# Kernel tuning notes

Measured on AMD Instinct MI355X. Metric: run time of the kernel, lower is better.

## Reference

```python
import jax, jax.numpy as jnp
import numpy as np

BATCH = 262144
N_STEPS = 10  # hard-coded `range(10)` in the original get_cycles


def _euler_to_matrix(e):
    # Standard extrinsic xyz convention: R = Rz(z) @ Ry(y) @ Rx(x)
    x, y, z = e[..., 0], e[..., 1], e[..., 2]
    cx, sx = jnp.cos(x), jnp.sin(x)
    cy, sy = jnp.cos(y), jnp.sin(y)
    cz, sz = jnp.cos(z), jnp.sin(z)
    r0 = jnp.stack([cz * cy, cz * sy * sx - sz * cx, cz * sy * cx + sz * sx], -1)
    r1 = jnp.stack([sz * cy, sz * sy * sx + cz * cx, sz * sy * cx - cz * sx], -1)
    r2 = jnp.stack([-sy, cy * sx, cy * cx], -1)
    return jnp.stack([r0, r1, r2], -2)  # (..., 3, 3)


def _matrix_to_euler(R):
    # Classic rotationMatrixToEulerAngles (inverse of Rz@Ry@Rx), with singular branch
    sy = jnp.sqrt(R[..., 0, 0] ** 2 + R[..., 1, 0] ** 2)
    singular = sy < 1e-6
    x = jnp.where(singular,
                  jnp.arctan2(-R[..., 1, 2], R[..., 1, 1]),
                  jnp.arctan2(R[..., 2, 1], R[..., 2, 2]))
    y = jnp.arctan2(-R[..., 2, 0], sy)
    z = jnp.where(singular, jnp.zeros_like(sy), jnp.arctan2(R[..., 1, 0], R[..., 0, 0]))
    return jnp.stack([x, y, z], -1)


def _get_cycles(x):
    # x: (B, 6*N_STEPS), interleaved [t(3), r(3)] per step (per the original reshape())
    x = jax.lax.stop_gradient(x)  # mirrors .detach().numpy() in the original
    g = x.reshape(x.shape[0], N_STEPS, 6)
    t = g[:, :, :3]   # (B, S, 3) translations
    r = g[:, :, 3:]   # (B, S, 3) euler rotations

    # --- translation part ---
    # The original aliases path_pred[0] onto t[0:3] via .numpy() and mutates it
    # in-place across cycle iterations (j=0 doubles it). The resulting recorded
    # values obey: v_0 = t_0 ; v_i = 2*v_{i-1} + sum_{j=1}^{i-1} t_j
    C = jnp.cumsum(t[:, 1:, :], axis=1)  # C[:, k-1, :] = sum_{j=1..k} t_j
    v = [t[:, 0, :]]
    for i in range(1, N_STEPS):
        tail = C[:, i - 2, :] if i >= 2 else jnp.zeros_like(v[0])
        v.append(2.0 * v[-1] + tail)
    trans = jnp.stack(v, axis=1)  # (B, S, 3)

    # --- rotation part ---
    # numpy `*=` is ELEMENTWISE, so cycle i records
    # matrix_to_euler( R(r_1) * prod_{j<i} R(r_j) )  (Hadamard product)
    R = _euler_to_matrix(r)                    # (B, S, 3, 3)
    CP = jnp.cumprod(R, axis=1)                # CP[:, k] = elemwise prod_{j<=k} R_j
    P = jnp.concatenate([jnp.ones_like(R[:, :1]), CP[:, :-1]], axis=1)  # prod_{j<i}
    M = R[:, 1:2] * P                          # (B, S, 3, 3)
    rot = _matrix_to_euler(M)                  # (B, S, 3)

    return jnp.stack([trans, rot], axis=2)     # (B, S, 2, 3)


def setup_inputs():
    key = jax.random.key(0)
    k1, k2 = jax.random.split(key)
    pred = jax.random.normal(k1, (BATCH, 6 * N_STEPS), dtype=jnp.float32)
    gt = jax.random.normal(k2, (BATCH, 6 * N_STEPS), dtype=jnp.float32)
    return {"pred": pred, "gt": gt}


def reference(pred, gt):
    pred_cycles = _get_cycles(pred)
    gt_cycles = _get_cycles(gt)
    loss = jnp.mean((pred_cycles - gt_cycles) ** 2)
    return loss / BATCH  # original divides the MSE by self.batch_size
```

## Files before the change

### kernel.cpp

```cpp
#include <hip/hip_runtime.h>
#include <math.h>

#define NSTEP 10
#define ROWS_PER_BLOCK 128
#define ROW_STRIDE 61
#define HALF_OFF (ROWS_PER_BLOCK * ROW_STRIDE)

__device__ __forceinline__ float fast_atan2f(float y, float x) {
    float ax = fabsf(x), ay = fabsf(y);
    float mx = fmaxf(ax, ay);
    float mn = fminf(ax, ay);
    float a = mn * __builtin_amdgcn_rcpf(fmaxf(mx, 1e-38f));
    float s = a * a;
    float r = fmaf(s, fmaf(s, fmaf(s, fmaf(s, 0.0208351f, -0.085133f),
                                   0.180141f), -0.3302995f), 0.9998660f) * a;
    if (ay > ax) r = 1.57079632679f - r;
    if (x < 0.0f) r = 3.14159265359f - r;
    return copysignf(r, y);
}

__device__ __forceinline__ void euler2mat(float x, float y, float z, float R[9]) {
    float sx, cx, sy, cy, sz, cz;
    __sincosf(x, &sx, &cx);
    __sincosf(y, &sy, &cy);
    __sincosf(z, &sz, &cz);
    R[0] = cz * cy; R[1] = cz * sy * sx - sz * cx; R[2] = cz * sy * cx + sz * sx;
    R[3] = sz * cy; R[4] = sz * sy * sx + cz * cx; R[5] = sz * sy * cx - cz * sx;
    R[6] = -sy;     R[7] = cy * sx;                R[8] = cy * cx;
}

__device__ __forceinline__ void emit(float v, float& acc) {
    int pi = __builtin_amdgcn_update_dpp(0, __float_as_int(v), 0xB1, 0xF, 0xF, true);
    float d = v - __int_as_float(pi);
    acc = fmaf(d, d, acc);
}

__device__ __forceinline__ void emit_euler(const float M[9], float& acc) {
    float sy = sqrtf(fmaf(M[0], M[0], M[3] * M[3]));
    bool sing = sy < 1e-6f;
    float a0 = sing ? -M[5] : M[7];
    float a1 = sing ?  M[4] : M[8];
    emit(fast_atan2f(a0, a1), acc);
    emit(fast_atan2f(-M[6], sy), acc);
    emit(sing ? 0.0f : fast_atan2f(M[3], M[0]), acc);
}

__global__ __launch_bounds__(256) void cycle_loss_main(
    const float* __restrict__ pred, const float* __restrict__ gt,
    float* __restrict__ partial, int batch)
{
    __shared__ float lds[2 * HALF_OFF];
    const int tid = threadIdx.x;

    {
        const size_t gbase = (size_t)blockIdx.x * (ROWS_PER_BLOCK * 60);
        #pragma unroll
        for (int it = 0; it < 30; ++it) {
            int i = tid + it * 256;
            int lidx = i + i / 60;
            lds[lidx]            = pred[gbase + i];
            lds[HALF_OFF + lidx] = gt[gbase + i];
        }
    }
    __syncthreads();

    float acc = 0.0f;
    {
        const float* row = lds + ((tid & 1) ? HALF_OFF : 0) + (tid >> 1) * ROW_STRIDE;

        float v[3], cac[3] = {0,0,0}, tprev[3];
        float Q[9];

        float e0 = row[0], e1 = row[1], e2 = row[2], e3 = row[3];
        float e4 = row[4], e5 = row[5], e6 = row[6], e7 = row[7];
        float e8 = row[8], e9 = row[9], e10 = row[10], e11 = row[11];

        v[0] = e0; v[1] = e1; v[2] = e2;
        emit(v[0], acc); emit(v[1], acc); emit(v[2], acc);
        #pragma unroll
        for (int k = 0; k < 3; ++k) { v[k] *= 2.0f; emit(v[k], acc); }
        tprev[0] = e6; tprev[1] = e7; tprev[2] = e8;

        {
            float R1[9];
            euler2mat(e3, e4, e5, Q);
            euler2mat(e9, e10, e11, R1);
            emit_euler(R1, acc);
            #pragma unroll
            for (int k = 0; k < 9; ++k) Q[k] *= R1[k];
            emit_euler(Q, acc);
            #pragma unroll
            for (int k = 0; k < 9; ++k) Q[k] *= R1[k];
        }

        #pragma unroll
        for (int c = 1; c < 5; ++c) {
            const float* rc = row + 12 * c;
            float f0 = rc[0], f1 = rc[1], f2 = rc[2], f3 = rc[3];
            float f4 = rc[4], f5 = rc[5], f6 = rc[6], f7 = rc[7];
            float f8 = rc[8], f9 = rc[9], f10 = rc[10], f11 = rc[11];

            cac[0] += tprev[0]; cac[1] += tprev[1]; cac[2] += tprev[2];
            #pragma unroll
            for (int k = 0; k < 3; ++k) { v[k] = fmaf(2.0f, v[k], cac[k]); emit(v[k], acc); }
            cac[0] += f0; cac[1] += f1; cac[2] += f2;
            #pragma unroll
            for (int k = 0; k < 3; ++k) { v[k] = fmaf(2.0f, v[k], cac[k]); emit(v[k], acc); }
            tprev[0] = f6; tprev[1] = f7; tprev[2] = f8;

            emit_euler(Q, acc);
            {
                float R[9];
                euler2mat(f3, f4, f5, R);
                #pragma unroll
                for (int k = 0; k < 9; ++k) Q[k] *= R[k];
            }
            emit_euler(Q, acc);
            if (c < 4) {
                float R[9];
                euler2mat(f9, f10, f11, R);
                #pragma unroll
                for (int k = 0; k < 9; ++k) Q[k] *= R[k];
            }
        }
    }

    int lane = tid & 63;
    int wid  = tid >> 6;
    #pragma unroll
    for (int off = 32; off > 0; off >>= 1)
        acc += __shfl_down(acc, off, 64);
    __shared__ float warp_s[4];
    if (lane == 0) warp_s[wid] = acc;
    __syncthreads();
    if (tid == 0)
        partial[blockIdx.x] = warp_s[0] + warp_s[1] + warp_s[2] + warp_s[3];
}

__global__ __launch_bounds__(256) void cycle_loss_fin(
    const float* __restrict__ partial, float* __restrict__ out,
    int nblocks, float inv)
{
    int t = threadIdx.x;
    float s = 0.0f;
    for (int i = t; i < nblocks; i += 256) s += partial[i];
    int lane = t & 63, wid = t >> 6;
    #pragma unroll
    for (int off = 32; off > 0; off >>= 1)
        s += __shfl_down(s, off, 64);
    __shared__ float warp_s[4];
    if (lane == 0) warp_s[wid] = s;
    __syncthreads();
    if (t == 0)
        out[0] = (warp_s[0] + warp_s[1] + warp_s[2] + warp_s[3]) * inv;
}

extern "C" void kernel_launch(void* const* d_in, const int* in_sizes, int n_in,
                              void* d_out, int out_size, void* d_ws, size_t ws_size,
                              hipStream_t stream) {
    const float* pred = (const float*)d_in[0];
    const float* gt   = (const float*)d_in[1];
    int batch = in_sizes[0] / 60;
    float* partial = (float*)d_ws;

    const int threads = 256;
    const int blocks = batch / ROWS_PER_BLOCK;
    cycle_loss_main<<<blocks, threads, 0, stream>>>(pred, gt, partial, batch);

    double inv = 0.5 / (60.0 * (double)batch * (double)batch);
    cycle_loss_fin<<<1, threads, 0, stream>>>(partial, (float*)d_out, blocks, (float)inv);
}
```

Baseline: 145.2 us.

## Stage inputs as packed fp16 in per-wave LDS tiles with float2 loads

Each wave now loads its own 32 rows of pred and gt with float2 global loads and converts them to packed half2 (round-toward-zero) before writing to LDS. This halves LDS footprint and LDS read count and allows more blocks per CU. The block-wide reduction barrier is replaced by per-wave partial sums written to global memory, and the final kernel sums four times as many partials. Storing inputs in fp16 loses precision, which is amplified by the doubling recurrence in the translation path and may break accuracy tolerance.

```diff
diff --git a/kernel.cpp b/kernel.cpp
--- a/kernel.cpp
+++ b/kernel.cpp
@@ -2,9 +2,11 @@
 #include <math.h>
 
 #define NSTEP 10
-#define ROWS_PER_BLOCK 128
-#define ROW_STRIDE 61
-#define HALF_OFF (ROWS_PER_BLOCK * ROW_STRIDE)
+#define ROW_U32 31
+#define GT_OFF  (32 * ROW_U32)
+#define WAVE_U32 (64 * ROW_U32)
+
+typedef __fp16 half2_t __attribute__((ext_vector_type(2)));
 
 __device__ __forceinline__ float fast_atan2f(float y, float x) {
     float ax = fabsf(x), ay = fabsf(y);
@@ -45,35 +47,55 @@
     emit(sing ? 0.0f : fast_atan2f(M[3], M[0]), acc);
 }
 
+__device__ __forceinline__ void unpack2(unsigned u, float& lo, float& hi) {
+    union { unsigned u; half2_t h; } cv; cv.u = u;
+    lo = (float)cv.h.x; hi = (float)cv.h.y;
+}
+
 __global__ __launch_bounds__(256) void cycle_loss_main(
     const float* __restrict__ pred, const float* __restrict__ gt,
-    float* __restrict__ partial, int batch)
+    float* __restrict__ partial)
 {
-    __shared__ float lds[2 * HALF_OFF];
-    const int tid = threadIdx.x;
+    __shared__ unsigned lds[4 * WAVE_U32];
+    const int tid  = threadIdx.x;
+    const int lane = tid & 63;
+    const int wid  = tid >> 6;
 
     {
-        const size_t gbase = (size_t)blockIdx.x * (ROWS_PER_BLOCK * 60);
+        const size_t rbase = ((size_t)blockIdx.x * 128 + wid * 32) * 30;
+        const float2* pp = reinterpret_cast<const float2*>(pred) + rbase;
+        const float2* gp = reinterpret_cast<const float2*>(gt)   + rbase;
+        unsigned* lw = lds + wid * WAVE_U32;
+
+        int cp  = lane % 30;
+        int idx = (lane / 30) * ROW_U32 + cp;
         #pragma unroll
-        for (int it = 0; it < 30; ++it) {
-            int i = tid + it * 256;
-            int lidx = i + i / 60;
-            lds[lidx]            = pred[gbase + i];
-            lds[HALF_OFF + lidx] = gt[gbase + i];
+        for (int it = 0; it < 15; ++it) {
+            float2 a = pp[lane + 64 * it];
+            float2 b = gp[lane + 64 * it];
+            half2_t ha = __builtin_amdgcn_cvt_pkrtz(a.x, a.y);
+            half2_t hb = __builtin_amdgcn_cvt_pkrtz(b.x, b.y);
+            union { half2_t h; unsigned u; } ca, cb; ca.h = ha; cb.h = hb;
+            lw[idx]          = ca.u;
+            lw[GT_OFF + idx] = cb.u;
+            idx += 2 * ROW_U32 + 4; cp += 4;
+            if (cp >= 30) { cp -= 30; idx += 1; }
         }
     }
     __syncthreads();
 
     float acc = 0.0f;
     {
-        const float* row = lds + ((tid & 1) ? HALF_OFF : 0) + (tid >> 1) * ROW_STRIDE;
+        const unsigned* row = lds + wid * WAVE_U32
+                            + ((lane & 1) ? GT_OFF : 0) + (lane >> 1) * ROW_U32;
 
         float v[3], cac[3] = {0,0,0}, tprev[3];
         float Q[9];
 
-        float e0 = row[0], e1 = row[1], e2 = row[2], e3 = row[3];
-        float e4 = row[4], e5 = row[5], e6 = row[6], e7 = row[7];
-        float e8 = row[8], e9 = row[9], e10 = row[10], e11 = row[11];
+        float e0,e1,e2,e3,e4,e5,e6,e7,e8,e9,e10,e11;
+        unpack2(row[0], e0, e1);  unpack2(row[1], e2, e3);
+        unpack2(row[2], e4, e5);  unpack2(row[3], e6, e7);
+        unpack2(row[4], e8, e9);  unpack2(row[5], e10, e11);
 
         v[0] = e0; v[1] = e1; v[2] = e2;
         emit(v[0], acc); emit(v[1], acc); emit(v[2], acc);
@@ -95,10 +117,11 @@
 
         #pragma unroll
         for (int c = 1; c < 5; ++c) {
-            const float* rc = row + 12 * c;
-            float f0 = rc[0], f1 = rc[1], f2 = rc[2], f3 = rc[3];
-            float f4 = rc[4], f5 = rc[5], f6 = rc[6], f7 = rc[7];
-            float f8 = rc[8], f9 = rc[9], f10 = rc[10], f11 = rc[11];
+            const unsigned* rc = row + 6 * c;
+            float f0,f1,f2,f3,f4,f5,f6,f7,f8,f9,f10,f11;
+            unpack2(rc[0], f0, f1);  unpack2(rc[1], f2, f3);
+            unpack2(rc[2], f4, f5);  unpack2(rc[3], f6, f7);
+            unpack2(rc[4], f8, f9);  unpack2(rc[5], f10, f11);
 
             cac[0] += tprev[0]; cac[1] += tprev[1]; cac[2] += tprev[2];
             #pragma unroll
@@ -125,25 +148,20 @@
         }
     }
 
-    int lane = tid & 63;
-    int wid  = tid >> 6;
     #pragma unroll
     for (int off = 32; off > 0; off >>= 1)
         acc += __shfl_down(acc, off, 64);
-    __shared__ float warp_s[4];
-    if (lane == 0) warp_s[wid] = acc;
-    __syncthreads();
-    if (tid == 0)
-        partial[blockIdx.x] = warp_s[0] + warp_s[1] + warp_s[2] + warp_s[3];
+    if (lane == 0)
+        partial[blockIdx.x * 4 + wid] = acc;
 }
 
 __global__ __launch_bounds__(256) void cycle_loss_fin(
     const float* __restrict__ partial, float* __restrict__ out,
-    int nblocks, float inv)
+    int nparts, float inv)
 {
     int t = threadIdx.x;
     float s = 0.0f;
-    for (int i = t; i < nblocks; i += 256) s += partial[i];
+    for (int i = t; i < nparts; i += 256) s += partial[i];
     int lane = t & 63, wid = t >> 6;
     #pragma unroll
     for (int off = 32; off > 0; off >>= 1)
@@ -164,9 +182,9 @@
     float* partial = (float*)d_ws;
 
     const int threads = 256;
-    const int blocks = batch / ROWS_PER_BLOCK;
-    cycle_loss_main<<<blocks, threads, 0, stream>>>(pred, gt, partial, batch);
+    const int blocks = batch / 128;
+    cycle_loss_main<<<blocks, threads, 0, stream>>>(pred, gt, partial);
 
     double inv = 0.5 / (60.0 * (double)batch * (double)batch);
-    cycle_loss_fin<<<1, threads, 0, stream>>>(partial, (float*)d_out, blocks, (float)inv);
+    cycle_loss_fin<<<1, threads, 0, stream>>>(partial, (float*)d_out, blocks * 4, (float)inv);
 }
```

New measurement: 150.3 us. 3.5% more time.
